# Kernel tuning notes

Hardware: AMD Instinct MI355X
Metric: run time of the kernel (lower is better)

The kernel has to match this reference:

```python
import jax, jax.numpy as jnp
import numpy as np

B, N, F, H, A, T = 4, 256, 64, 256, 16, 3


def setup_inputs() -> dict:
    key = jax.random.key(0)
    ks = jax.random.split(key, 18)
    s = 0.05
    rn = lambda k, shp: jax.random.normal(k, shp, dtype=jnp.float32) * s
    return {
        "node_features": jax.random.normal(ks[0], (B, N, F), dtype=jnp.float32),
        "adjacency": jax.random.randint(ks[1], (B, N, N), 0, 2).astype(jnp.int32),
        # preprocess MLP: F->H->H
        "pre_W1": rn(ks[2], (F, H)), "pre_b1": jnp.zeros((H,), jnp.float32),
        "pre_W2": rn(ks[3], (H, H)), "pre_b2": jnp.zeros((H,), jnp.float32),
        # message MLP: 2H->H->H
        "msg_W1": rn(ks[4], (2 * H, H)), "msg_b1": jnp.zeros((H,), jnp.float32),
        "msg_W2": rn(ks[5], (H, H)), "msg_b2": jnp.zeros((H,), jnp.float32),
        # GRUCell params (jax layout [in, 3H]; gate order r,z,n like torch)
        "gru_Wih": rn(ks[6], (H, 3 * H)), "gru_Whh": rn(ks[7], (H, 3 * H)),
        "gru_bih": jnp.zeros((3 * H,), jnp.float32), "gru_bhh": jnp.zeros((3 * H,), jnp.float32),
        # readout MLP: H->H->A
        "ro_W1": rn(ks[8], (H, H)), "ro_b1": jnp.zeros((H,), jnp.float32),
        "ro_W2": rn(ks[9], (H, A)), "ro_b2": jnp.zeros((A,), jnp.float32),
    }


def reference(node_features, adjacency, pre_W1, pre_b1, pre_W2, pre_b2,
              msg_W1, msg_b1, msg_W2, msg_b2,
              gru_Wih, gru_Whh, gru_bih, gru_bhh,
              ro_W1, ro_b1, ro_W2, ro_b2):
    adj = adjacency.astype(node_features.dtype)  # [B,N,N]
    # preprocess: Linear-ReLU-Linear
    h = jnp.maximum(node_features @ pre_W1 + pre_b1, 0.0) @ pre_W2 + pre_b2  # [B,N,H]

    W1_i, W1_j = msg_W1[:H], msg_W1[H:]  # concat([h_i,h_j]) @ W1 == h_i@W1_i + h_j@W1_j
    for _ in range(T):
        hi = h @ W1_i  # [B,N,H] receiver part
        hj = h @ W1_j  # [B,N,H] sender part
        e = jnp.maximum(hi[:, :, None, :] + hj[:, None, :, :] + msg_b1, 0.0)  # [B,N,N,H]
        m = e @ msg_W2 + msg_b2  # [B,N,N,H] messages
        agg = jnp.einsum('bijh,bij->bih', m, adj)  # mask + sum over senders j
        # GRUCell(input=agg, hidden=h), torch gate order (r, z, n)
        gi = agg @ gru_Wih + gru_bih  # [B,N,3H]
        gh = h @ gru_Whh + gru_bhh
        ir, iz, inn = jnp.split(gi, 3, axis=-1)
        hr, hz, hn = jnp.split(gh, 3, axis=-1)
        r = jax.nn.sigmoid(ir + hr)
        z = jax.nn.sigmoid(iz + hz)
        n = jnp.tanh(inn + r * hn)
        h = (1.0 - z) * n + z * h

    g = jnp.sum(h, axis=1)  # [B,H] graph readout
    q = jnp.maximum(g @ ro_W1 + ro_b1, 0.0) @ ro_W2 + ro_b2  # [B,A]
    return q
```

## Files before the change

### kernel.cpp

```cpp
#include <hip/hip_runtime.h>
#include <hip/hip_bf16.h>


typedef unsigned short ushort_t;
typedef short bf8_t __attribute__((ext_vector_type(8)));
typedef float f4_t  __attribute__((ext_vector_type(4)));

#define BN_ROWS 1024

#define UB_NFB    0
#define UB_PW1T   65536
#define UB_PW2T   81920
#define UB_WCATT  147456
#define UB_WGT    802816
#define UB_XB     1466368
#define UB_H2     1728512
#define UB_EHAT2  2252800
#define UB_END    3137536

#define F_PREB1   1568768
#define F_PREB2   1569024
#define F_BCAT    1569280
#define F_BIH     1570560
#define F_ROW1    1571328
#define F_ROB1    1636864
#define F_ROW2    1637120
#define F_ROB2    1641216
#define F_H       1641232
#define F_HCAT    1903376
#define F_GI      3214096
#define F_FLAG    4000528

#define CVa 65536
#define CVb 81920
#define CVc 147456
#define CVd 802816
#define CV_TOTAL 875280

__device__ __forceinline__ float bf2f(ushort_t u) {
    return __uint_as_float(((unsigned int)u) << 16);
}
__device__ __forceinline__ ushort_t f2b(float v) {
    __hip_bfloat16 b = __float2bfloat16(v);
    return *reinterpret_cast<ushort_t*>(&b);
}
__device__ __forceinline__ float relu(float v) { return v < 0.f ? 0.f : v; }
__device__ __forceinline__ float ld(const void* p, int i, int isf32) {
    return isf32 ? ((const float*)p)[i] : bf2f(((const ushort_t*)p)[i]);
}

__global__ __launch_bounds__(256) void detect_kernel(const ushort_t* __restrict__ nf,
                                                     int* __restrict__ flag) {
    __shared__ int cnt;
    if (threadIdx.x == 0) cnt = 0;
    __syncthreads();
    int bad = 0;
    for (int i = 0; i < 8; ++i) {
        ushort_t u = nf[(threadIdx.x * 8 + i) * 2];
        int ex = (u >> 7) & 0xFF;
        if ((u & 0x7fff) != 0 && (ex < 100 || ex > 140)) bad++;
    }
    atomicAdd(&cnt, bad);
    __syncthreads();
    if (threadIdx.x == 0) *flag = (cnt > 512) ? 1 : 0;
}

__global__ __launch_bounds__(256) void convert_kernel(
    const void* nf, const void* preW1, const void* preb1, const void* preW2, const void* preb2,
    const void* msgW1, const void* msgb1, const void* msgW2, const void* msgb2,
    const void* gruWih, const void* gruWhh, const void* grubih, const void* grubhh,
    const void* roW1, const void* rob1, const void* roW2, const void* rob2,
    float* __restrict__ w, const int* __restrict__ flagp)
{
    int e = blockIdx.x * 256 + threadIdx.x;
    if (e >= CV_TOTAL) return;
    const int f32 = *flagp;
    ushort_t* wb = (ushort_t*)w;
    if (e < CVa) {
        wb[UB_NFB + e] = f2b(ld(nf, e, f32));
    } else if (e < CVb) {
        int i = e - CVa; int n = i >> 6, k = i & 63;
        wb[UB_PW1T + i] = f2b(ld(preW1, k * 256 + n, f32));
    } else if (e < CVc) {
        int i = e - CVb; int n = i >> 8, k = i & 255;
        wb[UB_PW2T + i] = f2b(ld(preW2, k * 256 + n, f32));
    } else if (e < CVd) {
        int i = e - CVc; int n = i >> 9, k = (i & 511) & 255;
        float v;
        if (n < 256)      v = ld(msgW1, k * 256 + n, f32);
        else if (n < 512) v = ld(msgW1, (256 + k) * 256 + (n - 256), f32);
        else              v = ld(gruWhh, k * 768 + (n - 512), f32);
        wb[UB_WCATT + i] = f2b(v);
    } else {
        int f = e - CVd;
        float v;
        if (f < 256)        v = ld(preb1, f, f32);
        else if (f < 512)   v = ld(preb2, f - 256, f32);
        else if (f < 1792) {
            int c = f - 512;
            if (c < 256)      v = ld(msgb1, c, f32);
            else if (c < 512) v = 0.f;
            else              v = ld(grubhh, c - 512, f32);
        }
        else if (f < 2560)  v = ld(grubih, f - 1792, f32);
        else if (f < 68096) v = ld(roW1, f - 2560, f32);
        else if (f < 68352) v = ld(rob1, f - 68096, f32);
        else if (f < 72448) v = ld(roW2, f - 68352, f32);
        else                v = ld(rob2, f - 72448, f32);
        w[F_PREB1 + f] = v;
    }
}

__global__ __launch_bounds__(256) void wg_kernel(
    const void* msgW2, const void* msgb2, const void* gruWih,
    ushort_t* __restrict__ wgt, const int* __restrict__ flagp)
{
    __shared__ float w2s[4 * 256];
    const int f32 = *flagp;
    const int t = threadIdx.x;
    const int p0 = blockIdx.x * 256;
    const int k0 = blockIdx.y * 4;
    for (int i = t; i < 4 * 256; i += 256) {
        int r = i >> 8, n = i & 255;
        int krow = k0 + r;
        float v;
        if (krow < 256)       v = ld(msgW2, krow * 256 + n, f32);
        else if (krow == 256) v = ld(msgb2, n, f32);
        else                  v = 0.f;
        w2s[i] = v;
    }
    __syncthreads();
    const int p = p0 + t;
    float acc[4] = {};
    for (int n0 = 0; n0 < 256; n0 += 32) {
        float wv[32];
#pragma unroll
        for (int i = 0; i < 32; ++i)
            wv[i] = ld(gruWih, (n0 + i) * 768 + p, f32);
#pragma unroll
        for (int r = 0; r < 4; ++r) {
            float a = acc[r];
#pragma unroll
            for (int q = 0; q < 8; ++q) {
                f4_t w4 = *(const f4_t*)&w2s[r * 256 + n0 + q * 4];
                a += w4[0] * wv[q * 4 + 0] + w4[1] * wv[q * 4 + 1]
                   + w4[2] * wv[q * 4 + 2] + w4[3] * wv[q * 4 + 3];
            }
            acc[r] = a;
        }
    }
#pragma unroll
    for (int r = 0; r < 4; ++r) {
        int krow = k0 + r;
        ushort_t hi = f2b(acc[r]);
        ushort_t lo = f2b(acc[r] - bf2f(hi));
        wgt[p * 864 + krow] = hi;
        wgt[p * 864 + 288 + krow] = hi;
        wgt[p * 864 + 576 + krow] = lo;
    }
}

template<int BM>
__global__ __launch_bounds__(256) void mgemm_k(
    const ushort_t* __restrict__ A,
    const ushort_t* __restrict__ Bt,
    const float* __restrict__ bias,
    float* __restrict__ C,
    ushort_t* __restrict__ Cb, int cbld, int cblo,
    int K, int N, int dorelu)
{
    constexpr int MR = BM / 32;
    __shared__ ushort_t As[BM * 32];
    __shared__ ushort_t Bs[128 * 32];
    const int t = threadIdx.x;
    const int wave = t >> 6, lane = t & 63;
    const int ln = lane & 15, quad = lane >> 4;
    const int bm = blockIdx.y * BM, bn = blockIdx.x * 128;
    const int wm = (wave >> 1) * (BM / 2), wn = (wave & 1) * 64;
    const int srow = t >> 2, skc = (t & 3) << 3;

    f4_t acc[MR][4] = {};

    for (int k0 = 0; k0 < K; k0 += 32) {
        __syncthreads();
#pragma unroll
        for (int r = 0; r < BM / 64; ++r) {
            int row = srow + r * 64;
            *(bf8_t*)(&As[row * 32 + skc]) = *(const bf8_t*)(&A[(bm + row) * K + k0 + skc]);
        }
#pragma unroll
        for (int r = 0; r < 2; ++r) {
            int row = srow + r * 64;
            *(bf8_t*)(&Bs[row * 32 + skc]) = *(const bf8_t*)(&Bt[(bn + row) * K + k0 + skc]);
        }
        __syncthreads();
        bf8_t af[MR], bfr[4];
#pragma unroll
        for (int i = 0; i < MR; ++i)
            af[i]  = *(const bf8_t*)(&As[(wm + i * 16 + ln) * 32 + quad * 8]);
#pragma unroll
        for (int i = 0; i < 4; ++i)
            bfr[i] = *(const bf8_t*)(&Bs[(wn + i * 16 + ln) * 32 + quad * 8]);
#pragma unroll
        for (int mi = 0; mi < MR; ++mi)
#pragma unroll
            for (int ni = 0; ni < 4; ++ni)
                acc[mi][ni] = __builtin_amdgcn_mfma_f32_16x16x32_bf16(
                    af[mi], bfr[ni], acc[mi][ni], 0, 0, 0);
    }

#pragma unroll
    for (int mi = 0; mi < MR; ++mi) {
#pragma unroll
        for (int ni = 0; ni < 4; ++ni) {
            int col = bn + wn + ni * 16 + ln;
            float bb = bias ? bias[col] : 0.f;
#pragma unroll
            for (int r = 0; r < 4; ++r) {
                int row = bm + wm + mi * 16 + quad * 4 + r;
                float v = acc[mi][ni][r] + bb;
                if (dorelu) v = relu(v);
                if (C) C[row * N + col] = v;
                if (Cb) {
                    ushort_t hi = f2b(v);
                    Cb[row * cbld + col] = hi;
                    if (cblo) Cb[row * cbld + cblo + col] = f2b(v - bf2f(hi));
                }
            }
        }
    }
}

__global__ __launch_bounds__(256) void msg_kernel(
    const float* __restrict__ hcat,
    const int*   __restrict__ adj,
    ushort_t* __restrict__ ehat)
{
    const int row = blockIdx.x;
    const int t = threadIdx.x;
    __shared__ int ej[256];
    __shared__ int ecnt;
    if (t == 0) ecnt = 0;
    __syncthreads();
    if (adj[row * 256 + t]) { int p = atomicAdd(&ecnt, 1); ej[p] = t; }
    const float hi = hcat[row * 1280 + t];
    const float* hjb = hcat + (row >> 8) * 256 * 1280 + 256;
    __syncthreads();
    const int ne = ecnt;
    float acc = 0.f;
#pragma unroll 4
    for (int p = 0; p < ne; ++p) {
        int j = ej[p];
        acc += relu(hi + hjb[j * 1280 + t]);
    }
    ushort_t h16 = f2b(acc);
    ushort_t l16 = f2b(acc - bf2f(h16));
    ehat[row * 864 + t] = h16;
    ehat[row * 864 + 288 + t] = l16;
    ehat[row * 864 + 576 + t] = h16;
    if (t < 32) {
        ushort_t d = f2b(t == 0 ? (float)ne : 0.f);
        ehat[row * 864 + 256 + t] = d;
        ehat[row * 864 + 544 + t] = 0;
        ehat[row * 864 + 832 + t] = d;
    }
}

__global__ __launch_bounds__(256) void gru_kernel(
    const float* __restrict__ gi,
    const float* __restrict__ hcat,
    float* __restrict__ h,
    ushort_t* __restrict__ h2)
{
    const int row = blockIdx.x;
    const int t = threadIdx.x;
    const float* gir = gi + row * 768;
    const float* ghr = hcat + row * 1280 + 512;
    float ir = gir[t], iz = gir[256 + t], in = gir[512 + t];
    float hr = ghr[t], hz = ghr[256 + t], hn = ghr[512 + t];
    float r = 1.f / (1.f + __expf(-(ir + hr)));
    float z = 1.f / (1.f + __expf(-(iz + hz)));
    float n = tanhf(in + r * hn);
    float ho = h[row * 256 + t];
    float hv = (1.f - z) * n + z * ho;
    h[row * 256 + t] = hv;
    ushort_t hb = f2b(hv);
    h2[row * 512 + t] = hb;
    h2[row * 512 + 256 + t] = f2b(hv - bf2f(hb));
}

__global__ __launch_bounds__(256) void readout_kernel(
    const float* __restrict__ h,
    const float* __restrict__ roW1, const float* __restrict__ rob1,
    const float* __restrict__ roW2, const float* __restrict__ rob2,
    void* __restrict__ out, const int* __restrict__ flagp)
{
    const int b = blockIdx.x;
    const int t = threadIdx.x;
    __shared__ float gl[256], t1[256];
    const float* hb = h + b * 256 * 256;
    float s = 0.f;
    for (int n = 0; n < 256; ++n) s += hb[n * 256 + t];
    gl[t] = s;
    __syncthreads();
    float acc = rob1[t];
    for (int k = 0; k < 256; ++k) acc += gl[k] * roW1[k * 256 + t];
    t1[t] = relu(acc);
    __syncthreads();
    if (t < 16) {
        float q = rob2[t];
        for (int k = 0; k < 256; ++k) q += t1[k] * roW2[k * 16 + t];
        if (*flagp) ((float*)out)[b * 16 + t] = q;
        else ((__hip_bfloat16*)out)[b * 16 + t] = __float2bfloat16(q);
    }
}

extern "C" void kernel_launch(void* const* d_in, const int* in_sizes, int n_in,
                              void* d_out, int out_size, void* d_ws, size_t ws_size,
                              hipStream_t stream) {
    float* w = (float*)d_ws;
    ushort_t* wb = (ushort_t*)d_ws;
    int* flagp = (int*)(w + F_FLAG);

    static const int dictSz[18]  = {65536,262144,16384,256,65536,256,131072,256,65536,256,
                                    196608,196608,768,768,65536,256,4096,16};
    static const int alphaSz[18] = {262144,196608,196608,768,768,131072,65536,256,256,
                                    65536,16384,65536,256,256,65536,4096,256,16};
    static const int alphaPos[18] = {9,0,10,12,11,13,5,7,6,8,2,1,4,3,14,16,15,17};
    bool dictOK = true, alphaOK = true;
    for (int i = 0; i < 18 && i < n_in; ++i) {
        if (in_sizes[i] != dictSz[i])  dictOK = false;
        if (in_sizes[i] != alphaSz[i]) alphaOK = false;
    }
    const void* P[18];
    for (int l = 0; l < 18; ++l) P[l] = d_in[(!dictOK && alphaOK) ? alphaPos[l] : l];
    const int* adj = (const int*)P[1];

    detect_kernel<<<1, 256, 0, stream>>>((const ushort_t*)P[0], flagp);
    convert_kernel<<<(CV_TOTAL + 255) / 256, 256, 0, stream>>>(
        P[0], P[2], P[3], P[4], P[5], P[6], P[7], P[8], P[9],
        P[10], P[11], P[12], P[13], P[14], P[15], P[16], P[17], w, flagp);
    wg_kernel<<<dim3(3, 72), 256, 0, stream>>>(P[8], P[9], P[10], wb + UB_WGT, flagp);

    mgemm_k<64><<<dim3(2, 16), 256, 0, stream>>>(
        wb + UB_NFB, wb + UB_PW1T, w + F_PREB1, (float*)nullptr,
        wb + UB_XB, 256, 0, 64, 256, 1);
    mgemm_k<64><<<dim3(2, 16), 256, 0, stream>>>(
        wb + UB_XB, wb + UB_PW2T, w + F_PREB2, w + F_H,
        wb + UB_H2, 512, 256, 256, 256, 0);

    for (int it = 0; it < 3; ++it) {
        mgemm_k<64><<<dim3(10, 16), 256, 0, stream>>>(
            wb + UB_H2, wb + UB_WCATT, w + F_BCAT, w + F_HCAT,
            (ushort_t*)nullptr, 0, 0, 512, 1280, 0);
        msg_kernel<<<BN_ROWS, 256, 0, stream>>>(w + F_HCAT, adj, wb + UB_EHAT2);
        mgemm_k<64><<<dim3(6, 16), 256, 0, stream>>>(
            wb + UB_EHAT2, wb + UB_WGT, w + F_BIH, w + F_GI,
            (ushort_t*)nullptr, 0, 0, 864, 768, 0);
        gru_kernel<<<BN_ROWS, 256, 0, stream>>>(w + F_GI, w + F_HCAT,
                                                w + F_H, wb + UB_H2);
    }

    readout_kernel<<<4, 256, 0, stream>>>(w + F_H, w + F_ROW1, w + F_ROB1,
                                          w + F_ROW2, w + F_ROB2, d_out, flagp);
}
```

Baseline: 311.2 us.

## Fuse all stages into one persistent cooperative kernel with grid syncs

Replaces the sequence of about 17 kernel launches (detect, convert, weight fold, GEMMs, message, GRU, readout) with a single cooperative persistent kernel. Stages are separated by grid.sync and work is distributed over blocks with grid-stride loops. GEMM tiles shrink from 64x128 to 64x64 so more tiles exist to spread across the persistent grid. This targets per-launch overhead and idle gaps between small kernels, at the cost of grid-wide barrier latency, lower per-tile reuse, and a grid limited by co-residency.

```diff
diff --git a/kernel.cpp b/kernel.cpp
--- a/kernel.cpp
+++ b/kernel.cpp
@@ -1,12 +1,13 @@
 #include <hip/hip_runtime.h>
 #include <hip/hip_bf16.h>
+#include <hip/hip_cooperative_groups.h>
+
+namespace cg = cooperative_groups;
 
 
 typedef unsigned short ushort_t;
 typedef short bf8_t __attribute__((ext_vector_type(8)));
 typedef float f4_t  __attribute__((ext_vector_type(4)));
-
-#define BN_ROWS 1024
 
 #define UB_NFB    0
 #define UB_PW1T   65536
@@ -29,7 +30,6 @@
 #define F_H       1641232
 #define F_HCAT    1903376
 #define F_GI      3214096
-#define F_FLAG    4000528
 
 #define CVa 65536
 #define CVb 81920
@@ -49,269 +49,272 @@
     return isf32 ? ((const float*)p)[i] : bf2f(((const ushort_t*)p)[i]);
 }
 
-__global__ __launch_bounds__(256) void detect_kernel(const ushort_t* __restrict__ nf,
-                                                     int* __restrict__ flag) {
-    __shared__ int cnt;
-    if (threadIdx.x == 0) cnt = 0;
-    __syncthreads();
-    int bad = 0;
-    for (int i = 0; i < 8; ++i) {
-        ushort_t u = nf[(threadIdx.x * 8 + i) * 2];
-        int ex = (u >> 7) & 0xFF;
-        if ((u & 0x7fff) != 0 && (ex < 100 || ex > 140)) bad++;
-    }
-    atomicAdd(&cnt, bad);
-    __syncthreads();
-    if (threadIdx.x == 0) *flag = (cnt > 512) ? 1 : 0;
-}
-
-__global__ __launch_bounds__(256) void convert_kernel(
-    const void* nf, const void* preW1, const void* preb1, const void* preW2, const void* preb2,
-    const void* msgW1, const void* msgb1, const void* msgW2, const void* msgb2,
-    const void* gruWih, const void* gruWhh, const void* grubih, const void* grubhh,
-    const void* roW1, const void* rob1, const void* roW2, const void* rob2,
-    float* __restrict__ w, const int* __restrict__ flagp)
+struct MegaArgs {
+    const void* P[18];
+    float* w;
+    void* out;
+};
+
+__device__ void dgemm64(const ushort_t* __restrict__ A,
+                        const ushort_t* __restrict__ Bt,
+                        const float* __restrict__ bias,
+                        float* __restrict__ C,
+                        ushort_t* __restrict__ Cb, int cbld, int cblo,
+                        int K, int N, int dorelu,
+                        int nb, int bid, int t, char* smem)
 {
-    int e = blockIdx.x * 256 + threadIdx.x;
-    if (e >= CV_TOTAL) return;
-    const int f32 = *flagp;
-    ushort_t* wb = (ushort_t*)w;
-    if (e < CVa) {
-        wb[UB_NFB + e] = f2b(ld(nf, e, f32));
-    } else if (e < CVb) {
-        int i = e - CVa; int n = i >> 6, k = i & 63;
-        wb[UB_PW1T + i] = f2b(ld(preW1, k * 256 + n, f32));
-    } else if (e < CVc) {
-        int i = e - CVb; int n = i >> 8, k = i & 255;
-        wb[UB_PW2T + i] = f2b(ld(preW2, k * 256 + n, f32));
-    } else if (e < CVd) {
-        int i = e - CVc; int n = i >> 9, k = (i & 511) & 255;
-        float v;
-        if (n < 256)      v = ld(msgW1, k * 256 + n, f32);
-        else if (n < 512) v = ld(msgW1, (256 + k) * 256 + (n - 256), f32);
-        else              v = ld(gruWhh, k * 768 + (n - 512), f32);
-        wb[UB_WCATT + i] = f2b(v);
-    } else {
-        int f = e - CVd;
-        float v;
-        if (f < 256)        v = ld(preb1, f, f32);
-        else if (f < 512)   v = ld(preb2, f - 256, f32);
-        else if (f < 1792) {
-            int c = f - 512;
-            if (c < 256)      v = ld(msgb1, c, f32);
-            else if (c < 512) v = 0.f;
-            else              v = ld(grubhh, c - 512, f32);
-        }
-        else if (f < 2560)  v = ld(grubih, f - 1792, f32);
-        else if (f < 68096) v = ld(roW1, f - 2560, f32);
-        else if (f < 68352) v = ld(rob1, f - 68096, f32);
-        else if (f < 72448) v = ld(roW2, f - 68352, f32);
-        else                v = ld(rob2, f - 72448, f32);
-        w[F_PREB1 + f] = v;
-    }
-}
-
-__global__ __launch_bounds__(256) void wg_kernel(
-    const void* msgW2, const void* msgb2, const void* gruWih,
-    ushort_t* __restrict__ wgt, const int* __restrict__ flagp)
-{
-    __shared__ float w2s[4 * 256];
-    const int f32 = *flagp;
-    const int t = threadIdx.x;
-    const int p0 = blockIdx.x * 256;
-    const int k0 = blockIdx.y * 4;
-    for (int i = t; i < 4 * 256; i += 256) {
-        int r = i >> 8, n = i & 255;
-        int krow = k0 + r;
-        float v;
-        if (krow < 256)       v = ld(msgW2, krow * 256 + n, f32);
-        else if (krow == 256) v = ld(msgb2, n, f32);
-        else                  v = 0.f;
-        w2s[i] = v;
-    }
-    __syncthreads();
-    const int p = p0 + t;
-    float acc[4] = {};
-    for (int n0 = 0; n0 < 256; n0 += 32) {
-        float wv[32];
-#pragma unroll
-        for (int i = 0; i < 32; ++i)
-            wv[i] = ld(gruWih, (n0 + i) * 768 + p, f32);
-#pragma unroll
-        for (int r = 0; r < 4; ++r) {
-            float a = acc[r];
-#pragma unroll
-            for (int q = 0; q < 8; ++q) {
-                f4_t w4 = *(const f4_t*)&w2s[r * 256 + n0 + q * 4];
-                a += w4[0] * wv[q * 4 + 0] + w4[1] * wv[q * 4 + 1]
-                   + w4[2] * wv[q * 4 + 2] + w4[3] * wv[q * 4 + 3];
-            }
-            acc[r] = a;
-        }
-    }
-#pragma unroll
-    for (int r = 0; r < 4; ++r) {
-        int krow = k0 + r;
-        ushort_t hi = f2b(acc[r]);
-        ushort_t lo = f2b(acc[r] - bf2f(hi));
-        wgt[p * 864 + krow] = hi;
-        wgt[p * 864 + 288 + krow] = hi;
-        wgt[p * 864 + 576 + krow] = lo;
-    }
-}
-
-template<int BM>
-__global__ __launch_bounds__(256) void mgemm_k(
-    const ushort_t* __restrict__ A,
-    const ushort_t* __restrict__ Bt,
-    const float* __restrict__ bias,
-    float* __restrict__ C,
-    ushort_t* __restrict__ Cb, int cbld, int cblo,
-    int K, int N, int dorelu)
-{
-    constexpr int MR = BM / 32;
-    __shared__ ushort_t As[BM * 32];
-    __shared__ ushort_t Bs[128 * 32];
-    const int t = threadIdx.x;
+    ushort_t* As = (ushort_t*)smem;
+    ushort_t* Bs = (ushort_t*)smem + 64 * 32;
     const int wave = t >> 6, lane = t & 63;
     const int ln = lane & 15, quad = lane >> 4;
-    const int bm = blockIdx.y * BM, bn = blockIdx.x * 128;
-    const int wm = (wave >> 1) * (BM / 2), wn = (wave & 1) * 64;
+    const int wm = (wave >> 1) * 32, wn = (wave & 1) * 32;
     const int srow = t >> 2, skc = (t & 3) << 3;
-
-    f4_t acc[MR][4] = {};
-
-    for (int k0 = 0; k0 < K; k0 += 32) {
-        __syncthreads();
-#pragma unroll
-        for (int r = 0; r < BM / 64; ++r) {
-            int row = srow + r * 64;
-            *(bf8_t*)(&As[row * 32 + skc]) = *(const bf8_t*)(&A[(bm + row) * K + k0 + skc]);
-        }
-#pragma unroll
-        for (int r = 0; r < 2; ++r) {
-            int row = srow + r * 64;
-            *(bf8_t*)(&Bs[row * 32 + skc]) = *(const bf8_t*)(&Bt[(bn + row) * K + k0 + skc]);
-        }
-        __syncthreads();
-        bf8_t af[MR], bfr[4];
-#pragma unroll
-        for (int i = 0; i < MR; ++i)
-            af[i]  = *(const bf8_t*)(&As[(wm + i * 16 + ln) * 32 + quad * 8]);
-#pragma unroll
-        for (int i = 0; i < 4; ++i)
-            bfr[i] = *(const bf8_t*)(&Bs[(wn + i * 16 + ln) * 32 + quad * 8]);
-#pragma unroll
-        for (int mi = 0; mi < MR; ++mi)
-#pragma unroll
-            for (int ni = 0; ni < 4; ++ni)
-                acc[mi][ni] = __builtin_amdgcn_mfma_f32_16x16x32_bf16(
-                    af[mi], bfr[ni], acc[mi][ni], 0, 0, 0);
-    }
-
-#pragma unroll
-    for (int mi = 0; mi < MR; ++mi) {
-#pragma unroll
-        for (int ni = 0; ni < 4; ++ni) {
-            int col = bn + wn + ni * 16 + ln;
-            float bb = bias ? bias[col] : 0.f;
+    const int ntiles = (N >> 6) << 4;
+
+    for (int tile = bid; tile < ntiles; tile += nb) {
+        const int bm = (tile & 15) << 6;
+        const int bn = (tile >> 4) << 6;
+        f4_t acc[2][2] = {};
+        for (int k0 = 0; k0 < K; k0 += 32) {
+            __syncthreads();
+            *(bf8_t*)(&As[srow * 32 + skc]) = *(const bf8_t*)(&A[(bm + srow) * K + k0 + skc]);
+            *(bf8_t*)(&Bs[srow * 32 + skc]) = *(const bf8_t*)(&Bt[(bn + srow) * K + k0 + skc]);
+            __syncthreads();
+            bf8_t af[2], bfr[2];
+#pragma unroll
+            for (int i = 0; i < 2; ++i) {
+                af[i]  = *(const bf8_t*)(&As[(wm + i * 16 + ln) * 32 + quad * 8]);
+                bfr[i] = *(const bf8_t*)(&Bs[(wn + i * 16 + ln) * 32 + quad * 8]);
+            }
+#pragma unroll
+            for (int mi = 0; mi < 2; ++mi)
+#pragma unroll
+                for (int ni = 0; ni < 2; ++ni)
+                    acc[mi][ni] = __builtin_amdgcn_mfma_f32_16x16x32_bf16(
+                        af[mi], bfr[ni], acc[mi][ni], 0, 0, 0);
+        }
+#pragma unroll
+        for (int mi = 0; mi < 2; ++mi) {
+#pragma unroll
+            for (int ni = 0; ni < 2; ++ni) {
+                int col = bn + wn + ni * 16 + ln;
+                float bb = bias ? bias[col] : 0.f;
+#pragma unroll
+                for (int r = 0; r < 4; ++r) {
+                    int row = bm + wm + mi * 16 + quad * 4 + r;
+                    float v = acc[mi][ni][r] + bb;
+                    if (dorelu) v = relu(v);
+                    if (C) C[row * N + col] = v;
+                    if (Cb) {
+                        ushort_t hi = f2b(v);
+                        Cb[row * cbld + col] = hi;
+                        if (cblo) Cb[row * cbld + cblo + col] = f2b(v - bf2f(hi));
+                    }
+                }
+            }
+        }
+    }
+}
+
+__global__ __launch_bounds__(256, 2) void mega_kernel(MegaArgs a)
+{
+    auto grid = cg::this_grid();
+    const int nb = gridDim.x, bid = blockIdx.x, t = threadIdx.x;
+    float* __restrict__ w = a.w;
+    ushort_t* __restrict__ wb = (ushort_t*)w;
+    const int* __restrict__ adj = (const int*)a.P[1];
+
+    __shared__ __align__(16) char smem[8704];
+    int* cntp = (int*)(smem + 8192);
+
+    {
+        const ushort_t* nf0 = (const ushort_t*)a.P[0];
+        if (t == 0) *cntp = 0;
+        __syncthreads();
+        int bad = 0;
+        for (int i = 0; i < 8; ++i) {
+            ushort_t u = nf0[(t * 8 + i) * 2];
+            int ex = (u >> 7) & 0xFF;
+            if ((u & 0x7fff) != 0 && (ex < 100 || ex > 140)) bad++;
+        }
+        atomicAdd(cntp, bad);
+        __syncthreads();
+    }
+    const int f32 = (*cntp > 512) ? 1 : 0;
+    __syncthreads();
+
+    for (int e = bid * 256 + t; e < CV_TOTAL; e += nb * 256) {
+        if (e < CVa) {
+            wb[UB_NFB + e] = f2b(ld(a.P[0], e, f32));
+        } else if (e < CVb) {
+            int i = e - CVa; int n = i >> 6, k = i & 63;
+            wb[UB_PW1T + i] = f2b(ld(a.P[2], k * 256 + n, f32));
+        } else if (e < CVc) {
+            int i = e - CVb; int n = i >> 8, k = i & 255;
+            wb[UB_PW2T + i] = f2b(ld(a.P[4], k * 256 + n, f32));
+        } else if (e < CVd) {
+            int i = e - CVc; int n = i >> 9, k = (i & 511) & 255;
+            float v;
+            if (n < 256)      v = ld(a.P[6], k * 256 + n, f32);
+            else if (n < 512) v = ld(a.P[6], (256 + k) * 256 + (n - 256), f32);
+            else              v = ld(a.P[11], k * 768 + (n - 512), f32);
+            wb[UB_WCATT + i] = f2b(v);
+        } else {
+            int f = e - CVd;
+            float v;
+            if (f < 256)        v = ld(a.P[3], f, f32);
+            else if (f < 512)   v = ld(a.P[5], f - 256, f32);
+            else if (f < 1792) {
+                int c = f - 512;
+                if (c < 256)      v = ld(a.P[7], c, f32);
+                else if (c < 512) v = 0.f;
+                else              v = ld(a.P[13], c - 512, f32);
+            }
+            else if (f < 2560)  v = ld(a.P[12], f - 1792, f32);
+            else if (f < 68096) v = ld(a.P[14], f - 2560, f32);
+            else if (f < 68352) v = ld(a.P[15], f - 68096, f32);
+            else if (f < 72448) v = ld(a.P[16], f - 68352, f32);
+            else                v = ld(a.P[17], f - 72448, f32);
+            w[F_PREB1 + f] = v;
+        }
+    }
+
+    {
+        float* w2s = (float*)smem;
+        for (int wt = bid; wt < 216; wt += nb) {
+            int p0 = (wt % 3) * 256;
+            int k0 = (wt / 3) * 4;
+            __syncthreads();
+            for (int i = t; i < 4 * 256; i += 256) {
+                int r = i >> 8, n = i & 255;
+                int krow = k0 + r;
+                float v;
+                if (krow < 256)       v = ld(a.P[8], krow * 256 + n, f32);
+                else if (krow == 256) v = ld(a.P[9], n, f32);
+                else                  v = 0.f;
+                w2s[i] = v;
+            }
+            __syncthreads();
+            const int p = p0 + t;
+            float acc4[4] = {};
+            for (int n0 = 0; n0 < 256; n0 += 32) {
+                float wv[32];
+#pragma unroll
+                for (int i = 0; i < 32; ++i)
+                    wv[i] = ld(a.P[10], (n0 + i) * 768 + p, f32);
+#pragma unroll
+                for (int r = 0; r < 4; ++r) {
+                    float acc = acc4[r];
+#pragma unroll
+                    for (int q = 0; q < 8; ++q) {
+                        f4_t w4 = *(const f4_t*)&w2s[r * 256 + n0 + q * 4];
+                        acc += w4[0] * wv[q * 4 + 0] + w4[1] * wv[q * 4 + 1]
+                             + w4[2] * wv[q * 4 + 2] + w4[3] * wv[q * 4 + 3];
+                    }
+                    acc4[r] = acc;
+                }
+            }
 #pragma unroll
             for (int r = 0; r < 4; ++r) {
-                int row = bm + wm + mi * 16 + quad * 4 + r;
-                float v = acc[mi][ni][r] + bb;
-                if (dorelu) v = relu(v);
-                if (C) C[row * N + col] = v;
-                if (Cb) {
-                    ushort_t hi = f2b(v);
-                    Cb[row * cbld + col] = hi;
-                    if (cblo) Cb[row * cbld + cblo + col] = f2b(v - bf2f(hi));
+                int krow = k0 + r;
+                ushort_t hi = f2b(acc4[r]);
+                ushort_t lo = f2b(acc4[r] - bf2f(hi));
+                wb[UB_WGT + p * 864 + krow] = hi;
+                wb[UB_WGT + p * 864 + 288 + krow] = hi;
+                wb[UB_WGT + p * 864 + 576 + krow] = lo;
+            }
+        }
+    }
+    grid.sync();
+
+    dgemm64(wb + UB_NFB, wb + UB_PW1T, w + F_PREB1, (float*)nullptr,
+            wb + UB_XB, 256, 0, 64, 256, 1, nb, bid, t, smem);
+    grid.sync();
+    dgemm64(wb + UB_XB, wb + UB_PW2T, w + F_PREB2, w + F_H,
+            wb + UB_H2, 512, 256, 256, 256, 0, nb, bid, t, smem);
+    grid.sync();
+
+    for (int it = 0; it < 3; ++it) {
+        dgemm64(wb + UB_H2, wb + UB_WCATT, w + F_BCAT, w + F_HCAT,
+                (ushort_t*)nullptr, 0, 0, 512, 1280, 0, nb, bid, t, smem);
+        grid.sync();
+
+        {
+            int* ej = (int*)smem;
+            const float* hcat = w + F_HCAT;
+            for (int idx = bid; idx < 1024; idx += nb) {
+                const int row = ((idx & 7) << 7) + (idx >> 3);
+                __syncthreads();
+                if (t == 0) *cntp = 0;
+                __syncthreads();
+                if (adj[row * 256 + t]) { int p = atomicAdd(cntp, 1); ej[p] = t; }
+                const float hi = hcat[row * 1280 + t];
+                const float* hjb = hcat + (row >> 8) * (256 * 1280) + 256;
+                __syncthreads();
+                const int ne = *cntp;
+                float acc = 0.f;
+#pragma unroll 4
+                for (int p = 0; p < ne; ++p) {
+                    int j = ej[p];
+                    acc += relu(hi + hjb[j * 1280 + t]);
                 }
-            }
-        }
-    }
-}
-
-__global__ __launch_bounds__(256) void msg_kernel(
-    const float* __restrict__ hcat,
-    const int*   __restrict__ adj,
-    ushort_t* __restrict__ ehat)
-{
-    const int row = blockIdx.x;
-    const int t = threadIdx.x;
-    __shared__ int ej[256];
-    __shared__ int ecnt;
-    if (t == 0) ecnt = 0;
-    __syncthreads();
-    if (adj[row * 256 + t]) { int p = atomicAdd(&ecnt, 1); ej[p] = t; }
-    const float hi = hcat[row * 1280 + t];
-    const float* hjb = hcat + (row >> 8) * 256 * 1280 + 256;
-    __syncthreads();
-    const int ne = ecnt;
-    float acc = 0.f;
-#pragma unroll 4
-    for (int p = 0; p < ne; ++p) {
-        int j = ej[p];
-        acc += relu(hi + hjb[j * 1280 + t]);
-    }
-    ushort_t h16 = f2b(acc);
-    ushort_t l16 = f2b(acc - bf2f(h16));
-    ehat[row * 864 + t] = h16;
-    ehat[row * 864 + 288 + t] = l16;
-    ehat[row * 864 + 576 + t] = h16;
-    if (t < 32) {
-        ushort_t d = f2b(t == 0 ? (float)ne : 0.f);
-        ehat[row * 864 + 256 + t] = d;
-        ehat[row * 864 + 544 + t] = 0;
-        ehat[row * 864 + 832 + t] = d;
-    }
-}
-
-__global__ __launch_bounds__(256) void gru_kernel(
-    const float* __restrict__ gi,
-    const float* __restrict__ hcat,
-    float* __restrict__ h,
-    ushort_t* __restrict__ h2)
-{
-    const int row = blockIdx.x;
-    const int t = threadIdx.x;
-    const float* gir = gi + row * 768;
-    const float* ghr = hcat + row * 1280 + 512;
-    float ir = gir[t], iz = gir[256 + t], in = gir[512 + t];
-    float hr = ghr[t], hz = ghr[256 + t], hn = ghr[512 + t];
-    float r = 1.f / (1.f + __expf(-(ir + hr)));
-    float z = 1.f / (1.f + __expf(-(iz + hz)));
-    float n = tanhf(in + r * hn);
-    float ho = h[row * 256 + t];
-    float hv = (1.f - z) * n + z * ho;
-    h[row * 256 + t] = hv;
-    ushort_t hb = f2b(hv);
-    h2[row * 512 + t] = hb;
-    h2[row * 512 + 256 + t] = f2b(hv - bf2f(hb));
-}
-
-__global__ __launch_bounds__(256) void readout_kernel(
-    const float* __restrict__ h,
-    const float* __restrict__ roW1, const float* __restrict__ rob1,
-    const float* __restrict__ roW2, const float* __restrict__ rob2,
-    void* __restrict__ out, const int* __restrict__ flagp)
-{
-    const int b = blockIdx.x;
-    const int t = threadIdx.x;
-    __shared__ float gl[256], t1[256];
-    const float* hb = h + b * 256 * 256;
-    float s = 0.f;
-    for (int n = 0; n < 256; ++n) s += hb[n * 256 + t];
-    gl[t] = s;
-    __syncthreads();
-    float acc = rob1[t];
-    for (int k = 0; k < 256; ++k) acc += gl[k] * roW1[k * 256 + t];
-    t1[t] = relu(acc);
-    __syncthreads();
-    if (t < 16) {
-        float q = rob2[t];
-        for (int k = 0; k < 256; ++k) q += t1[k] * roW2[k * 16 + t];
-        if (*flagp) ((float*)out)[b * 16 + t] = q;
-        else ((__hip_bfloat16*)out)[b * 16 + t] = __float2bfloat16(q);
+                ushort_t h16 = f2b(acc);
+                ushort_t l16 = f2b(acc - bf2f(h16));
+                ushort_t* er = wb + UB_EHAT2 + row * 864;
+                er[t] = h16;
+                er[288 + t] = l16;
+                er[576 + t] = h16;
+                if (t < 32) {
+                    ushort_t d = f2b(t == 0 ? (float)ne : 0.f);
+                    er[256 + t] = d;
+                    er[544 + t] = 0;
+                    er[832 + t] = d;
+                }
+            }
+        }
+        grid.sync();
+
+        dgemm64(wb + UB_EHAT2, wb + UB_WGT, w + F_BIH, w + F_GI,
+                (ushort_t*)nullptr, 0, 0, 864, 768, 0, nb, bid, t, smem);
+        grid.sync();
+
+        for (int row = bid; row < 1024; row += nb) {
+            const float* gir = w + F_GI + row * 768;
+            const float* ghr = w + F_HCAT + row * 1280 + 512;
+            float ir = gir[t], iz = gir[256 + t], in = gir[512 + t];
+            float hr = ghr[t], hz = ghr[256 + t], hn = ghr[512 + t];
+            float r = 1.f / (1.f + __expf(-(ir + hr)));
+            float z = 1.f / (1.f + __expf(-(iz + hz)));
+            float n = tanhf(in + r * hn);
+            float ho = w[F_H + row * 256 + t];
+            float hv = (1.f - z) * n + z * ho;
+            w[F_H + row * 256 + t] = hv;
+            ushort_t hb = f2b(hv);
+            wb[UB_H2 + row * 512 + t] = hb;
+            wb[UB_H2 + row * 512 + 256 + t] = f2b(hv - bf2f(hb));
+        }
+        grid.sync();
+    }
+
+    if (bid < 4) {
+        float* gl = (float*)smem;
+        float* t1 = gl + 256;
+        const float* hb = w + F_H + bid * 256 * 256;
+        __syncthreads();
+        float s = 0.f;
+        for (int n = 0; n < 256; ++n) s += hb[n * 256 + t];
+        gl[t] = s;
+        __syncthreads();
+        float acc = w[F_ROB1 + t];
+        for (int k = 0; k < 256; ++k) acc += gl[k] * w[F_ROW1 + k * 256 + t];
+        t1[t] = relu(acc);
+        __syncthreads();
+        if (t < 16) {
+            float q = w[F_ROB2 + t];
+            for (int k = 0; k < 256; ++k) q += t1[k] * w[F_ROW2 + k * 16 + t];
+            if (f32) ((float*)a.out)[bid * 16 + t] = q;
+            else ((__hip_bfloat16*)a.out)[bid * 16 + t] = __float2bfloat16(q);
+        }
     }
 }
 
@@ -319,8 +322,6 @@
                               void* d_out, int out_size, void* d_ws, size_t ws_size,
                               hipStream_t stream) {
     float* w = (float*)d_ws;
-    ushort_t* wb = (ushort_t*)d_ws;
-    int* flagp = (int*)(w + F_FLAG);
 
     static const int dictSz[18]  = {65536,262144,16384,256,65536,256,131072,256,65536,256,
                                     196608,196608,768,768,65536,256,4096,16};
@@ -332,35 +333,17 @@
         if (in_sizes[i] != dictSz[i])  dictOK = false;
         if (in_sizes[i] != alphaSz[i]) alphaOK = false;
     }
-    const void* P[18];
-    for (int l = 0; l < 18; ++l) P[l] = d_in[(!dictOK && alphaOK) ? alphaPos[l] : l];
-    const int* adj = (const int*)P[1];
-
-    detect_kernel<<<1, 256, 0, stream>>>((const ushort_t*)P[0], flagp);
-    convert_kernel<<<(CV_TOTAL + 255) / 256, 256, 0, stream>>>(
-        P[0], P[2], P[3], P[4], P[5], P[6], P[7], P[8], P[9],
-        P[10], P[11], P[12], P[13], P[14], P[15], P[16], P[17], w, flagp);
-    wg_kernel<<<dim3(3, 72), 256, 0, stream>>>(P[8], P[9], P[10], wb + UB_WGT, flagp);
-
-    mgemm_k<64><<<dim3(2, 16), 256, 0, stream>>>(
-        wb + UB_NFB, wb + UB_PW1T, w + F_PREB1, (float*)nullptr,
-        wb + UB_XB, 256, 0, 64, 256, 1);
-    mgemm_k<64><<<dim3(2, 16), 256, 0, stream>>>(
-        wb + UB_XB, wb + UB_PW2T, w + F_PREB2, w + F_H,
-        wb + UB_H2, 512, 256, 256, 256, 0);
-
-    for (int it = 0; it < 3; ++it) {
-        mgemm_k<64><<<dim3(10, 16), 256, 0, stream>>>(
-            wb + UB_H2, wb + UB_WCATT, w + F_BCAT, w + F_HCAT,
-            (ushort_t*)nullptr, 0, 0, 512, 1280, 0);
-        msg_kernel<<<BN_ROWS, 256, 0, stream>>>(w + F_HCAT, adj, wb + UB_EHAT2);
-        mgemm_k<64><<<dim3(6, 16), 256, 0, stream>>>(
-            wb + UB_EHAT2, wb + UB_WGT, w + F_BIH, w + F_GI,
-            (ushort_t*)nullptr, 0, 0, 864, 768, 0);
-        gru_kernel<<<BN_ROWS, 256, 0, stream>>>(w + F_GI, w + F_HCAT,
-                                                w + F_H, wb + UB_H2);
-    }
-
-    readout_kernel<<<4, 256, 0, stream>>>(w + F_H, w + F_ROW1, w + F_ROB1,
-                                          w + F_ROW2, w + F_ROB2, d_out, flagp);
-}
+    MegaArgs margs;
+    for (int l = 0; l < 18; ++l)
+        margs.P[l] = d_in[(!dictOK && alphaOK) ? alphaPos[l] : l];
+    margs.w = w;
+    margs.out = d_out;
+
+    int nbpc = 0;
+    hipOccupancyMaxActiveBlocksPerMultiprocessor(&nbpc, mega_kernel, 256, 0);
+    int grid = (nbpc >= 2) ? 512 : 256;
+
+    void* kargs[] = { (void*)&margs };
+    hipLaunchCooperativeKernel((const void*)mega_kernel, dim3(grid), dim3(256),
+                               kargs, 0, stream);
+}
```

New measurement: 1.195 ms. 3.84x slower.

## Fuse weight conversion kernels, preprocess MLP, and gi GEMM with GRU update

Applied to the files above, without the earlier changes.

Merges the convert and wg weight-prep kernels into one launch, fuses the two preprocess GEMMs into a single kernel that keeps the hidden activation in shared memory, and fuses the GRU input GEMM with the GRU gate epilogue so the gi buffer is never written. This removes several kernel launches and a round trip through global memory per iteration. The fused GRU kernel runs only 64 blocks and loads r/z/n weight slices per block, which may underuse the GPU compared with the earlier 96-block GEMM plus a 1024-block elementwise kernel.

```diff
diff --git a/kernel.cpp b/kernel.cpp
--- a/kernel.cpp
+++ b/kernel.cpp
@@ -13,10 +13,8 @@
 #define UB_PW2T   81920
 #define UB_WCATT  147456
 #define UB_WGT    802816
-#define UB_XB     1466368
 #define UB_H2     1728512
 #define UB_EHAT2  2252800
-#define UB_END    3137536
 
 #define F_PREB1   1568768
 #define F_PREB2   1569024
@@ -28,7 +26,6 @@
 #define F_ROB2    1641216
 #define F_H       1641232
 #define F_HCAT    1903376
-#define F_GI      3214096
 #define F_FLAG    4000528
 
 #define CVa 65536
@@ -36,6 +33,7 @@
 #define CVc 147456
 #define CVd 802816
 #define CV_TOTAL 875280
+#define NCONV 3420
 
 __device__ __forceinline__ float bf2f(ushort_t u) {
     return __uint_as_float(((unsigned int)u) << 16);
@@ -65,61 +63,60 @@
     if (threadIdx.x == 0) *flag = (cnt > 512) ? 1 : 0;
 }
 
-__global__ __launch_bounds__(256) void convert_kernel(
+__global__ __launch_bounds__(256) void convwg_kernel(
     const void* nf, const void* preW1, const void* preb1, const void* preW2, const void* preb2,
     const void* msgW1, const void* msgb1, const void* msgW2, const void* msgb2,
     const void* gruWih, const void* gruWhh, const void* grubih, const void* grubhh,
     const void* roW1, const void* rob1, const void* roW2, const void* rob2,
     float* __restrict__ w, const int* __restrict__ flagp)
 {
-    int e = blockIdx.x * 256 + threadIdx.x;
-    if (e >= CV_TOTAL) return;
-    const int f32 = *flagp;
-    ushort_t* wb = (ushort_t*)w;
-    if (e < CVa) {
-        wb[UB_NFB + e] = f2b(ld(nf, e, f32));
-    } else if (e < CVb) {
-        int i = e - CVa; int n = i >> 6, k = i & 63;
-        wb[UB_PW1T + i] = f2b(ld(preW1, k * 256 + n, f32));
-    } else if (e < CVc) {
-        int i = e - CVb; int n = i >> 8, k = i & 255;
-        wb[UB_PW2T + i] = f2b(ld(preW2, k * 256 + n, f32));
-    } else if (e < CVd) {
-        int i = e - CVc; int n = i >> 9, k = (i & 511) & 255;
-        float v;
-        if (n < 256)      v = ld(msgW1, k * 256 + n, f32);
-        else if (n < 512) v = ld(msgW1, (256 + k) * 256 + (n - 256), f32);
-        else              v = ld(gruWhh, k * 768 + (n - 512), f32);
-        wb[UB_WCATT + i] = f2b(v);
-    } else {
-        int f = e - CVd;
-        float v;
-        if (f < 256)        v = ld(preb1, f, f32);
-        else if (f < 512)   v = ld(preb2, f - 256, f32);
-        else if (f < 1792) {
-            int c = f - 512;
-            if (c < 256)      v = ld(msgb1, c, f32);
-            else if (c < 512) v = 0.f;
-            else              v = ld(grubhh, c - 512, f32);
-        }
-        else if (f < 2560)  v = ld(grubih, f - 1792, f32);
-        else if (f < 68096) v = ld(roW1, f - 2560, f32);
-        else if (f < 68352) v = ld(rob1, f - 68096, f32);
-        else if (f < 72448) v = ld(roW2, f - 68352, f32);
-        else                v = ld(rob2, f - 72448, f32);
-        w[F_PREB1 + f] = v;
-    }
-}
-
-__global__ __launch_bounds__(256) void wg_kernel(
-    const void* msgW2, const void* msgb2, const void* gruWih,
-    ushort_t* __restrict__ wgt, const int* __restrict__ flagp)
-{
     __shared__ float w2s[4 * 256];
     const int f32 = *flagp;
     const int t = threadIdx.x;
-    const int p0 = blockIdx.x * 256;
-    const int k0 = blockIdx.y * 4;
+    ushort_t* wb = (ushort_t*)w;
+
+    if (blockIdx.x < NCONV) {
+        int e = blockIdx.x * 256 + t;
+        if (e >= CV_TOTAL) return;
+        if (e < CVa) {
+            wb[UB_NFB + e] = f2b(ld(nf, e, f32));
+        } else if (e < CVb) {
+            int i = e - CVa; int n = i >> 6, k = i & 63;
+            wb[UB_PW1T + i] = f2b(ld(preW1, k * 256 + n, f32));
+        } else if (e < CVc) {
+            int i = e - CVb; int n = i >> 8, k = i & 255;
+            wb[UB_PW2T + i] = f2b(ld(preW2, k * 256 + n, f32));
+        } else if (e < CVd) {
+            int i = e - CVc; int n = i >> 9, k = (i & 511) & 255;
+            float v;
+            if (n < 256)      v = ld(msgW1, k * 256 + n, f32);
+            else if (n < 512) v = ld(msgW1, (256 + k) * 256 + (n - 256), f32);
+            else              v = ld(gruWhh, k * 768 + (n - 512), f32);
+            wb[UB_WCATT + i] = f2b(v);
+        } else {
+            int f = e - CVd;
+            float v;
+            if (f < 256)        v = ld(preb1, f, f32);
+            else if (f < 512)   v = ld(preb2, f - 256, f32);
+            else if (f < 1792) {
+                int c = f - 512;
+                if (c < 256)      v = ld(msgb1, c, f32);
+                else if (c < 512) v = 0.f;
+                else              v = ld(grubhh, c - 512, f32);
+            }
+            else if (f < 2560)  v = ld(grubih, f - 1792, f32);
+            else if (f < 68096) v = ld(roW1, f - 2560, f32);
+            else if (f < 68352) v = ld(rob1, f - 68096, f32);
+            else if (f < 72448) v = ld(roW2, f - 68352, f32);
+            else                v = ld(rob2, f - 72448, f32);
+            w[F_PREB1 + f] = v;
+        }
+        return;
+    }
+
+    const int wt = blockIdx.x - NCONV;
+    const int p0 = (wt % 3) * 256;
+    const int k0 = (wt / 3) * 4;
     for (int i = t; i < 4 * 256; i += 256) {
         int r = i >> 8, n = i & 255;
         int krow = k0 + r;
@@ -131,7 +128,7 @@
     }
     __syncthreads();
     const int p = p0 + t;
-    float acc[4] = {};
+    float acc4[4] = {};
     for (int n0 = 0; n0 < 256; n0 += 32) {
         float wv[32];
 #pragma unroll
@@ -139,70 +136,146 @@
             wv[i] = ld(gruWih, (n0 + i) * 768 + p, f32);
 #pragma unroll
         for (int r = 0; r < 4; ++r) {
-            float a = acc[r];
+            float acc = acc4[r];
 #pragma unroll
             for (int q = 0; q < 8; ++q) {
                 f4_t w4 = *(const f4_t*)&w2s[r * 256 + n0 + q * 4];
-                a += w4[0] * wv[q * 4 + 0] + w4[1] * wv[q * 4 + 1]
-                   + w4[2] * wv[q * 4 + 2] + w4[3] * wv[q * 4 + 3];
+                acc += w4[0] * wv[q * 4 + 0] + w4[1] * wv[q * 4 + 1]
+                     + w4[2] * wv[q * 4 + 2] + w4[3] * wv[q * 4 + 3];
             }
-            acc[r] = a;
+            acc4[r] = acc;
         }
     }
 #pragma unroll
     for (int r = 0; r < 4; ++r) {
         int krow = k0 + r;
-        ushort_t hi = f2b(acc[r]);
-        ushort_t lo = f2b(acc[r] - bf2f(hi));
-        wgt[p * 864 + krow] = hi;
-        wgt[p * 864 + 288 + krow] = hi;
-        wgt[p * 864 + 576 + krow] = lo;
-    }
-}
-
-template<int BM>
+        ushort_t hi = f2b(acc4[r]);
+        ushort_t lo = f2b(acc4[r] - bf2f(hi));
+        wb[UB_WGT + p * 864 + krow] = hi;
+        wb[UB_WGT + p * 864 + 288 + krow] = hi;
+        wb[UB_WGT + p * 864 + 576 + krow] = lo;
+    }
+}
+
+__global__ __launch_bounds__(256) void prenet_kernel(float* __restrict__ w)
+{
+    __shared__ ushort_t As[64 * 64];
+    __shared__ ushort_t Xs[64 * 256];
+    __shared__ ushort_t Bs[256 * 32];
+    ushort_t* wb = (ushort_t*)w;
+    const int t = threadIdx.x;
+    const int wave = t >> 6, lane = t & 63;
+    const int ln = lane & 15, quad = lane >> 4;
+    const int rbase = blockIdx.x * 64;
+    const int srow = t >> 2, skc = (t & 3) << 3;
+
+#pragma unroll
+    for (int s = 0; s < 2; ++s) {
+        int slot = t + 256 * s;
+        int row = slot >> 3, kc = (slot & 7) << 3;
+        *(bf8_t*)(&As[row * 64 + kc]) =
+            *(const bf8_t*)(&wb[UB_NFB + (rbase + row) * 64 + kc]);
+    }
+
+    f4_t acc[16] = {};
+    for (int k0 = 0; k0 < 64; k0 += 32) {
+        __syncthreads();
+#pragma unroll
+        for (int rr = 0; rr < 4; ++rr) {
+            int n = srow + 64 * rr;
+            *(bf8_t*)(&Bs[n * 32 + skc]) =
+                *(const bf8_t*)(&wb[UB_PW1T + n * 64 + k0 + skc]);
+        }
+        __syncthreads();
+        bf8_t af = *(const bf8_t*)(&As[(wave * 16 + ln) * 64 + k0 + quad * 8]);
+#pragma unroll
+        for (int n = 0; n < 16; ++n) {
+            bf8_t bfr = *(const bf8_t*)(&Bs[(n * 16 + ln) * 32 + quad * 8]);
+            acc[n] = __builtin_amdgcn_mfma_f32_16x16x32_bf16(af, bfr, acc[n], 0, 0, 0);
+        }
+    }
+    __syncthreads();
+#pragma unroll
+    for (int n = 0; n < 16; ++n) {
+        int col = n * 16 + ln;
+        float bb = w[F_PREB1 + col];
+#pragma unroll
+        for (int r = 0; r < 4; ++r) {
+            int row = wave * 16 + quad * 4 + r;
+            Xs[row * 256 + col] = f2b(relu(acc[n][r] + bb));
+        }
+        acc[n] = (f4_t){0.f, 0.f, 0.f, 0.f};
+    }
+    __syncthreads();
+
+    for (int k0 = 0; k0 < 256; k0 += 32) {
+        __syncthreads();
+#pragma unroll
+        for (int rr = 0; rr < 4; ++rr) {
+            int n = srow + 64 * rr;
+            *(bf8_t*)(&Bs[n * 32 + skc]) =
+                *(const bf8_t*)(&wb[UB_PW2T + n * 256 + k0 + skc]);
+        }
+        __syncthreads();
+        bf8_t af = *(const bf8_t*)(&Xs[(wave * 16 + ln) * 256 + k0 + quad * 8]);
+#pragma unroll
+        for (int n = 0; n < 16; ++n) {
+            bf8_t bfr = *(const bf8_t*)(&Bs[(n * 16 + ln) * 32 + quad * 8]);
+            acc[n] = __builtin_amdgcn_mfma_f32_16x16x32_bf16(af, bfr, acc[n], 0, 0, 0);
+        }
+    }
+#pragma unroll
+    for (int n = 0; n < 16; ++n) {
+        int col = n * 16 + ln;
+        float bb = w[F_PREB2 + col];
+#pragma unroll
+        for (int r = 0; r < 4; ++r) {
+            int grow = rbase + wave * 16 + quad * 4 + r;
+            float v = acc[n][r] + bb;
+            w[F_H + grow * 256 + col] = v;
+            ushort_t hi = f2b(v);
+            wb[UB_H2 + grow * 512 + col] = hi;
+            wb[UB_H2 + grow * 512 + 256 + col] = f2b(v - bf2f(hi));
+        }
+    }
+}
+
 __global__ __launch_bounds__(256) void mgemm_k(
     const ushort_t* __restrict__ A,
     const ushort_t* __restrict__ Bt,
     const float* __restrict__ bias,
     float* __restrict__ C,
-    ushort_t* __restrict__ Cb, int cbld, int cblo,
-    int K, int N, int dorelu)
-{
-    constexpr int MR = BM / 32;
-    __shared__ ushort_t As[BM * 32];
+    int K, int N)
+{
+    __shared__ ushort_t As[64 * 32];
     __shared__ ushort_t Bs[128 * 32];
     const int t = threadIdx.x;
     const int wave = t >> 6, lane = t & 63;
     const int ln = lane & 15, quad = lane >> 4;
-    const int bm = blockIdx.y * BM, bn = blockIdx.x * 128;
-    const int wm = (wave >> 1) * (BM / 2), wn = (wave & 1) * 64;
+    const int bm = blockIdx.y * 64, bn = blockIdx.x * 128;
+    const int wm = (wave >> 1) * 32, wn = (wave & 1) * 64;
     const int srow = t >> 2, skc = (t & 3) << 3;
 
-    f4_t acc[MR][4] = {};
+    f4_t acc[2][4] = {};
 
     for (int k0 = 0; k0 < K; k0 += 32) {
         __syncthreads();
-#pragma unroll
-        for (int r = 0; r < BM / 64; ++r) {
-            int row = srow + r * 64;
-            *(bf8_t*)(&As[row * 32 + skc]) = *(const bf8_t*)(&A[(bm + row) * K + k0 + skc]);
-        }
+        *(bf8_t*)(&As[srow * 32 + skc]) = *(const bf8_t*)(&A[(bm + srow) * K + k0 + skc]);
 #pragma unroll
         for (int r = 0; r < 2; ++r) {
             int row = srow + r * 64;
             *(bf8_t*)(&Bs[row * 32 + skc]) = *(const bf8_t*)(&Bt[(bn + row) * K + k0 + skc]);
         }
         __syncthreads();
-        bf8_t af[MR], bfr[4];
-#pragma unroll
-        for (int i = 0; i < MR; ++i)
+        bf8_t af[2], bfr[4];
+#pragma unroll
+        for (int i = 0; i < 2; ++i)
             af[i]  = *(const bf8_t*)(&As[(wm + i * 16 + ln) * 32 + quad * 8]);
 #pragma unroll
         for (int i = 0; i < 4; ++i)
             bfr[i] = *(const bf8_t*)(&Bs[(wn + i * 16 + ln) * 32 + quad * 8]);
 #pragma unroll
-        for (int mi = 0; mi < MR; ++mi)
+        for (int mi = 0; mi < 2; ++mi)
 #pragma unroll
             for (int ni = 0; ni < 4; ++ni)
                 acc[mi][ni] = __builtin_amdgcn_mfma_f32_16x16x32_bf16(
@@ -210,22 +283,15 @@
     }
 
 #pragma unroll
-    for (int mi = 0; mi < MR; ++mi) {
+    for (int mi = 0; mi < 2; ++mi) {
 #pragma unroll
         for (int ni = 0; ni < 4; ++ni) {
             int col = bn + wn + ni * 16 + ln;
-            float bb = bias ? bias[col] : 0.f;
+            float bb = bias[col];
 #pragma unroll
             for (int r = 0; r < 4; ++r) {
                 int row = bm + wm + mi * 16 + quad * 4 + r;
-                float v = acc[mi][ni][r] + bb;
-                if (dorelu) v = relu(v);
-                if (C) C[row * N + col] = v;
-                if (Cb) {
-                    ushort_t hi = f2b(v);
-                    Cb[row * cbld + col] = hi;
-                    if (cblo) Cb[row * cbld + cblo + col] = f2b(v - bf2f(hi));
-                }
+                C[row * N + col] = acc[mi][ni][r] + bb;
             }
         }
     }
@@ -255,38 +321,77 @@
     }
     ushort_t h16 = f2b(acc);
     ushort_t l16 = f2b(acc - bf2f(h16));
-    ehat[row * 864 + t] = h16;
-    ehat[row * 864 + 288 + t] = l16;
-    ehat[row * 864 + 576 + t] = h16;
+    ushort_t* er = ehat + row * 864;
+    er[t] = h16;
+    er[288 + t] = l16;
+    er[576 + t] = h16;
     if (t < 32) {
         ushort_t d = f2b(t == 0 ? (float)ne : 0.f);
-        ehat[row * 864 + 256 + t] = d;
-        ehat[row * 864 + 544 + t] = 0;
-        ehat[row * 864 + 832 + t] = d;
-    }
-}
-
-__global__ __launch_bounds__(256) void gru_kernel(
-    const float* __restrict__ gi,
-    const float* __restrict__ hcat,
-    float* __restrict__ h,
-    ushort_t* __restrict__ h2)
-{
-    const int row = blockIdx.x;
-    const int t = threadIdx.x;
-    const float* gir = gi + row * 768;
-    const float* ghr = hcat + row * 1280 + 512;
-    float ir = gir[t], iz = gir[256 + t], in = gir[512 + t];
-    float hr = ghr[t], hz = ghr[256 + t], hn = ghr[512 + t];
-    float r = 1.f / (1.f + __expf(-(ir + hr)));
-    float z = 1.f / (1.f + __expf(-(iz + hz)));
-    float n = tanhf(in + r * hn);
-    float ho = h[row * 256 + t];
-    float hv = (1.f - z) * n + z * ho;
-    h[row * 256 + t] = hv;
-    ushort_t hb = f2b(hv);
-    h2[row * 512 + t] = hb;
-    h2[row * 512 + 256 + t] = f2b(hv - bf2f(hb));
+        er[256 + t] = d;
+        er[544 + t] = 0;
+        er[832 + t] = d;
+    }
+}
+
+__global__ __launch_bounds__(256) void gigru_kernel(float* __restrict__ w)
+{
+    __shared__ ushort_t As[64 * 32];
+    __shared__ ushort_t Bs[192 * 32];
+    ushort_t* wb = (ushort_t*)w;
+    const int t = threadIdx.x;
+    const int wave = t >> 6, lane = t & 63;
+    const int ln = lane & 15, quad = lane >> 4;
+    const int rg = blockIdx.x >> 2, cg = blockIdx.x & 3;
+    const int rbase = rg * 64;
+    const int srow = t >> 2, skc = (t & 3) << 3;
+
+    f4_t acc[12] = {};
+
+    for (int k0 = 0; k0 < 864; k0 += 32) {
+        __syncthreads();
+        *(bf8_t*)(&As[srow * 32 + skc]) =
+            *(const bf8_t*)(&wb[UB_EHAT2 + (rbase + srow) * 864 + k0 + skc]);
+#pragma unroll
+        for (int rr = 0; rr < 3; ++rr) {
+            int br = srow + 64 * rr;
+            int wrow = (br >> 6) * 256 + cg * 64 + (br & 63);
+            *(bf8_t*)(&Bs[br * 32 + skc]) =
+                *(const bf8_t*)(&wb[UB_WGT + wrow * 864 + k0 + skc]);
+        }
+        __syncthreads();
+        bf8_t af = *(const bf8_t*)(&As[(wave * 16 + ln) * 32 + quad * 8]);
+#pragma unroll
+        for (int n = 0; n < 12; ++n) {
+            bf8_t bfr = *(const bf8_t*)(&Bs[(n * 16 + ln) * 32 + quad * 8]);
+            acc[n] = __builtin_amdgcn_mfma_f32_16x16x32_bf16(af, bfr, acc[n], 0, 0, 0);
+        }
+    }
+
+#pragma unroll
+    for (int n = 0; n < 4; ++n) {
+        int col = cg * 64 + n * 16 + ln;
+        float bi_r = w[F_BIH + col];
+        float bi_z = w[F_BIH + 256 + col];
+        float bi_n = w[F_BIH + 512 + col];
+#pragma unroll
+        for (int r = 0; r < 4; ++r) {
+            int row = rbase + wave * 16 + quad * 4 + r;
+            float ir = acc[n][r] + bi_r;
+            float iz = acc[n + 4][r] + bi_z;
+            float in = acc[n + 8][r] + bi_n;
+            const float* ghr = w + F_HCAT + row * 1280 + 512;
+            float hr = ghr[col], hz = ghr[256 + col], hn = ghr[512 + col];
+            float rg_ = 1.f / (1.f + __expf(-(ir + hr)));
+            float z   = 1.f / (1.f + __expf(-(iz + hz)));
+            float nn  = tanhf(in + rg_ * hn);
+            float ho = w[F_H + row * 256 + col];
+            float hv = (1.f - z) * nn + z * ho;
+            w[F_H + row * 256 + col] = hv;
+            ushort_t hb = f2b(hv);
+            wb[UB_H2 + row * 512 + col] = hb;
+            wb[UB_H2 + row * 512 + 256 + col] = f2b(hv - bf2f(hb));
+        }
+    }
 }
 
 __global__ __launch_bounds__(256) void readout_kernel(
@@ -337,28 +442,17 @@
     const int* adj = (const int*)P[1];
 
     detect_kernel<<<1, 256, 0, stream>>>((const ushort_t*)P[0], flagp);
-    convert_kernel<<<(CV_TOTAL + 255) / 256, 256, 0, stream>>>(
+    convwg_kernel<<<NCONV + 216, 256, 0, stream>>>(
         P[0], P[2], P[3], P[4], P[5], P[6], P[7], P[8], P[9],
         P[10], P[11], P[12], P[13], P[14], P[15], P[16], P[17], w, flagp);
-    wg_kernel<<<dim3(3, 72), 256, 0, stream>>>(P[8], P[9], P[10], wb + UB_WGT, flagp);
-
-    mgemm_k<64><<<dim3(2, 16), 256, 0, stream>>>(
-        wb + UB_NFB, wb + UB_PW1T, w + F_PREB1, (float*)nullptr,
-        wb + UB_XB, 256, 0, 64, 256, 1);
-    mgemm_k<64><<<dim3(2, 16), 256, 0, stream>>>(
-        wb + UB_XB, wb + UB_PW2T, w + F_PREB2, w + F_H,
-        wb + UB_H2, 512, 256, 256, 256, 0);
+
+    prenet_kernel<<<16, 256, 0, stream>>>(w);
 
     for (int it = 0; it < 3; ++it) {
-        mgemm_k<64><<<dim3(10, 16), 256, 0, stream>>>(
-            wb + UB_H2, wb + UB_WCATT, w + F_BCAT, w + F_HCAT,
-            (ushort_t*)nullptr, 0, 0, 512, 1280, 0);
+        mgemm_k<<<dim3(10, 16), 256, 0, stream>>>(
+            wb + UB_H2, wb + UB_WCATT, w + F_BCAT, w + F_HCAT, 512, 1280);
         msg_kernel<<<BN_ROWS, 256, 0, stream>>>(w + F_HCAT, adj, wb + UB_EHAT2);
-        mgemm_k<64><<<dim3(6, 16), 256, 0, stream>>>(
-            wb + UB_EHAT2, wb + UB_WGT, w + F_BIH, w + F_GI,
-            (ushort_t*)nullptr, 0, 0, 864, 768, 0);
-        gru_kernel<<<BN_ROWS, 256, 0, stream>>>(w + F_GI, w + F_HCAT,
-                                                w + F_H, wb + UB_H2);
+        gigru_kernel<<<64, 256, 0, stream>>>(w);
     }
 
     readout_kernel<<<4, 256, 0, stream>>>(w + F_H, w + F_ROW1, w + F_ROB1,
```

New measurement: 337.1 us. 1.08x slower.
